# Performance work log

Hardware: AMD Instinct MI355X
Metric: run time of the kernel (lower is better)

Reference implementation:

```python
import jax, jax.numpy as jnp
import numpy as np

NUM_EMBEDDINGS = 8192
EMBEDDING_DIM = 128
COMMITMENT_COST = 0.02


def _l2_normalize(x, axis=-1, eps=1e-12):
    # matches torch F.normalize: x / max(||x||, eps)
    n = jnp.sqrt(jnp.sum(x * x, axis=axis, keepdims=True))
    return x / jnp.maximum(n, eps)


def setup_inputs() -> dict:
    key = jax.random.key(0)
    k1, k2 = jax.random.split(key)
    inputs = jax.random.normal(k1, (16, 128, 2048), dtype=jnp.float32)  # [B, D, T]
    lim = 1.0 / NUM_EMBEDDINGS
    codebook = jax.random.uniform(k2, (NUM_EMBEDDINGS, EMBEDDING_DIM),
                                  dtype=jnp.float32, minval=-lim, maxval=lim)
    return {"inputs": inputs, "codebook": codebook}


def reference(inputs, codebook):
    # inputs: [B, D, T] -> [B, T, D]
    x = jnp.transpose(inputs, (0, 2, 1))
    B, T, D = x.shape
    flat = x.reshape(-1, D)                      # [N, D]
    flat_n = _l2_normalize(flat, axis=1)         # [N, D]
    emb_n = _l2_normalize(codebook, axis=1)      # [K, D]
    # cosine-style distance: 2 - 2 * <x_hat, e_hat>
    distances = 2.0 - 2.0 * jnp.einsum('nd,kd->nk', flat_n, emb_n)  # [N, K]
    encoding_indices = jnp.argmin(distances, axis=1)[:, None]       # [N, 1]
    # (dead-code revival is a training-time RNG side effect on the codebook;
    #  eval path / reference math skips it)
    quantized = codebook[encoding_indices[:, 0]].reshape(B, T, D)   # [B, T, D]
    sg = jax.lax.stop_gradient
    e_latent_loss = jnp.mean((sg(quantized) - x) ** 2)
    q_latent_loss = jnp.mean((quantized - sg(x)) ** 2)
    loss = q_latent_loss + COMMITMENT_COST * e_latent_loss
    # straight-through estimator
    quantized_st = x + sg(quantized - x)
    out = jnp.transpose(quantized_st, (0, 2, 1))  # back to [B, D, T]
    return loss, out, encoding_indices
```

## Files before the change

### kernel.cpp

```cpp
#include <hip/hip_runtime.h>
#include <hip/hip_bf16.h>

#define NROWS 32768
#define KCODES 8192
#define DDIM 128
#define TT 2048
#define ETOT 4194304

typedef __attribute__((ext_vector_type(8))) _Float16 f16x8;
typedef __attribute__((ext_vector_type(4))) float f32x4;

__device__ __forceinline__ float pk(float v, int p) {
    return __int_as_float((__float_as_int(v) & 0xFFFFE000) | p);
}

__device__ __forceinline__ void async16(char* lds_uniform, const char* g_perlane) {
    __builtin_amdgcn_global_load_lds(
        (const __attribute__((address_space(1))) unsigned int*)g_perlane,
        (__attribute__((address_space(3))) unsigned int*)lds_uniform,
        16, 0, 0);
}

#define SYNC2 asm volatile("s_waitcnt vmcnt(2) lgkmcnt(0)\n\ts_barrier" ::: "memory")
#define SYNC0 asm volatile("s_waitcnt vmcnt(0) lgkmcnt(0)\n\ts_barrier" ::: "memory")

__global__ void k_prep(const float* __restrict__ cb, _Float16* __restrict__ eh,
                       const float* __restrict__ in, _Float16* __restrict__ xh) {
    __shared__ float tb[64][65];
    int bid = blockIdx.x;
    if (bid < 2048) {
        int w = (bid * blockDim.x + threadIdx.x) >> 6;
        int l = threadIdx.x & 63;
        if (w >= KCODES) return;
        const float* row = cb + (long)w * DDIM;
        float v0 = row[l], v1 = row[l + 64];
        float ss = v0 * v0 + v1 * v1;
#pragma unroll
        for (int s = 1; s < 64; s <<= 1) ss += __shfl_xor(ss, s, 64);
        float inv = 1.0f / fmaxf(sqrtf(ss), 1e-12f);
        int tile = w >> 4, c = w & 15;
#pragma unroll
        for (int e = 0; e < 2; e++) {
            int d = l + e * 64;
            float v = (e ? v1 : v0) * inv;
            int ks = d >> 5, kq = (d >> 3) & 3, dr = d & 7;
            long off = (long)tile * 2048 + ks * 512 + (kq * 16 + c) * 8 + dr;
            eh[off] = (_Float16)v;
        }
    } else {
        bid -= 2048;
        int tt0 = (bid & 31) * 64;
        int dd0 = ((bid >> 5) & 1) * 64;
        int b = bid >> 6;
        const float* base = in + (long)b * DDIM * TT;
        int tl = threadIdx.x & 63;
        int dg = threadIdx.x >> 6;
#pragma unroll
        for (int i = 0; i < 16; i++) {
            int dd = dg + i * 4;
            tb[dd][tl] = base[(long)(dd0 + dd) * TT + tt0 + tl];
        }
        __syncthreads();
        int dl = threadIdx.x & 63;
        int tg = threadIdx.x >> 6;
#pragma unroll
        for (int i = 0; i < 16; i++) {
            int t = tg + i * 4;
            long n = (long)b * TT + tt0 + t;
            xh[n * DDIM + dd0 + dl] = (_Float16)tb[dl][t];
        }
    }
}

__device__ __forceinline__ void mfma4i(const char* buf, int l,
                                       const f16x8 (&bx)[4][4], f32x4 (&acc)[4]) {
    const f32x4 Z = {0.f, 0.f, 0.f, 0.f};
    f16x8 ah[4];
#pragma unroll
    for (int ks = 0; ks < 4; ks++)
        ah[ks] = *(const f16x8*)(buf + ks * 1024 + l * 16);
    __builtin_amdgcn_s_setprio(1);
#pragma unroll
    for (int nf = 0; nf < 4; nf++)
        acc[nf] = __builtin_amdgcn_mfma_f32_16x16x32_f16(ah[0], bx[nf][0], Z, 0, 0, 0);
#pragma unroll
    for (int ks = 1; ks < 4; ks++)
#pragma unroll
        for (int nf = 0; nf < 4; nf++)
            acc[nf] = __builtin_amdgcn_mfma_f32_16x16x32_f16(ah[ks], bx[nf][ks], acc[nf], 0, 0, 0);
    __builtin_amdgcn_s_setprio(0);
}

__device__ __forceinline__ void sel4(const f32x4 (&acc)[4], int PP,
                                     float (&t1)[4], float (&t2)[4], float (&u1)[4]) {
#pragma unroll
    for (int nf = 0; nf < 4; nf++) {
        f32x4 a = acc[nf];
        float s0 = pk(a[0], PP),     s1 = pk(a[1], PP - 1);
        float s2 = pk(a[2], PP - 2), s3 = pk(a[3], PP - 3);
        float h01 = fmaxf(s0, s1), l01 = fminf(s0, s1);
        float h23 = fmaxf(s2, s3), l23 = fminf(s2, s3);
        float m1 = fmaxf(h01, h23);
        float m2 = fmaxf(fminf(h01, h23), fmaxf(l01, l23));
        float n1 = fminf(t1[nf], m1); t1[nf] = fmaxf(t1[nf], m1);
        t2[nf] = fmaxf(t2[nf], n1);
        u1[nf] = fmaxf(u1[nf], m2);
    }
}

__global__ __launch_bounds__(256, 3) void k_main(const _Float16* __restrict__ xh,
                                                 const _Float16* __restrict__ eh,
                                                 int* __restrict__ cand) {
    extern __shared__ char lds[];
    const int tid = threadIdx.x;
    const int l = tid & 63;
    const int w = tid >> 6;
    const int e8 = blockIdx.x & 7;
    const int rb = blockIdx.x >> 3;
    const int col = l & 15, kq = l >> 4;
    const long rbase = (long)rb * 256;

    f16x8 bx[4][4];
#pragma unroll
    for (int nf = 0; nf < 4; nf++) {
        long n = rbase + w * 64 + nf * 16 + col;
#pragma unroll
        for (int ks = 0; ks < 4; ks++)
            bx[nf][ks] = *(const f16x8*)(xh + n * DDIM + ks * 32 + kq * 8);
    }

    const float NEG = __int_as_float(0xFF800000);
    float t1[4], t2[4], u1[4];
#pragma unroll
    for (int i = 0; i < 4; i++) { t1[i] = t2[i] = u1[i] = NEG; }

    int P = 8191 - (e8 * 1024 + kq * 4);

    const char* gsrc = (const char*)eh + (long)e8 * 262144 + w * 1024 + l * 16;
    char* b0 = lds;
    char* b1 = lds + 8192;
    char* b2 = lds + 16384;

    async16(b0 + w * 1024, gsrc);
    async16(b0 + 4096 + w * 1024, gsrc + 4096);
    async16(b1 + w * 1024, gsrc + 8192);
    async16(b1 + 4096 + w * 1024, gsrc + 12288);

    f32x4 accA[4], accB[4];
    int PA, PB;

    SYNC2;
    async16(b2 + w * 1024, gsrc + 2 * 8192);
    async16(b2 + 4096 + w * 1024, gsrc + 2 * 8192 + 4096);
    mfma4i(b0, l, bx, accA); PA = P; P -= 16;
    mfma4i(b0 + 4096, l, bx, accB); PB = P; P -= 16;
    sel4(accA, PA, t1, t2, u1);
    { char* tp = b0; b0 = b1; b1 = b2; b2 = tp; }

    for (int p = 1; p <= 30; ++p) {
        SYNC2;
        if (p < 30) {
            async16(b2 + w * 1024, gsrc + (long)(p + 2) * 8192);
            async16(b2 + 4096 + w * 1024, gsrc + (long)(p + 2) * 8192 + 4096);
        }
        mfma4i(b0, l, bx, accA); PA = P; P -= 16;
        sel4(accB, PB, t1, t2, u1);
        mfma4i(b0 + 4096, l, bx, accB); PB = P; P -= 16;
        sel4(accA, PA, t1, t2, u1);
        { char* tp = b0; b0 = b1; b1 = b2; b2 = tp; }
    }
    SYNC0;
    mfma4i(b0, l, bx, accA); PA = P; P -= 16;
    sel4(accB, PB, t1, t2, u1);
    mfma4i(b0 + 4096, l, bx, accB); PB = P;
    sel4(accA, PA, t1, t2, u1);
    sel4(accB, PB, t1, t2, u1);

    __syncthreads();
    float* mrg = (float*)lds;
#pragma unroll
    for (int nf = 0; nf < 4; nf++) {
        int row = w * 64 + nf * 16 + col;
        int e = kq * 3;
        mrg[row * 13 + e + 0] = t1[nf];
        mrg[row * 13 + e + 1] = t2[nf];
        mrg[row * 13 + e + 2] = u1[nf];
    }
    __syncthreads();
    {
        float s1 = NEG, s2 = NEG;
#pragma unroll 4
        for (int e = 0; e < 12; e++) {
            float v = mrg[tid * 13 + e];
            float a1 = fminf(s1, v); s1 = fmaxf(s1, v);
            s2 = fmaxf(s2, a1);
        }
        long n = rbase + tid;
        int* cp = cand + n * 16 + e8 * 2;
        cp[0] = 8191 - (__float_as_int(s1) & 0x1FFF);
        cp[1] = 8191 - (__float_as_int(s2) & 0x1FFF);
    }
}

__global__ void k_rf(const float* __restrict__ in, const float* __restrict__ cb,
                     const int* __restrict__ cand, float* __restrict__ out,
                     float* __restrict__ idx_f, double* __restrict__ part) {
    __shared__ float xs[16][132];
    __shared__ int sbi[16];
    __shared__ double sd[256];
    const int tid = threadIdx.x;
    const int n0 = blockIdx.x * 16;
    const int b = n0 >> 11, t0 = n0 & 2047;

    {
        int d = tid >> 1, h = tid & 1;
        const float* src = in + ((long)b * DDIM + d) * TT + t0 + h * 8;
        float4 v0 = *(const float4*)src;
        float4 v1 = *(const float4*)(src + 4);
#pragma unroll
        for (int j = 0; j < 4; j++) {
            xs[h * 8 + j][d] = ((const float*)&v0)[j];
            xs[h * 8 + 4 + j][d] = ((const float*)&v1)[j];
        }
    }
    __syncthreads();

    {
        int r = tid >> 4, k = tid & 15;
        int n = n0 + r;
        int c = cand[n * 16 + k];
        const float4* e = (const float4*)(cb + (long)c * DDIM);
        double dot = 0.0, nrm = 0.0;
        for (int d4 = 0; d4 < 32; d4++) {
            float4 q = e[d4];
#pragma unroll
            for (int j = 0; j < 4; j++) {
                double xd = (double)xs[r][d4 * 4 + j];
                double f = (double)((const float*)&q)[j];
                dot += xd * f;
                nrm += f * f;
            }
        }
        double sv = dot / fmax(sqrt(nrm), 1e-12);
#pragma unroll
        for (int s = 1; s < 16; s <<= 1) {
            double osv = __shfl_xor(sv, s, 64);
            int oc = __shfl_xor(c, s, 64);
            if (osv > sv || (osv == sv && oc < c)) { sv = osv; c = oc; }
        }
        if (k == 0) {
            sbi[r] = c;
            idx_f[n] = (float)c;
        }
    }
    __syncthreads();

    {
        int d = tid >> 1, h = tid & 1;
        float* ob = out + ((long)b * DDIM + d) * TT + t0 + h * 8;
        double acc = 0.0;
        float ov[8];
#pragma unroll
        for (int j = 0; j < 8; j++) {
            int rr = h * 8 + j;
            float xv = xs[rr][d];
            float qv = cb[(long)sbi[rr] * DDIM + d];
            float diff = qv - xv;
            ov[j] = xv + diff;
            acc += (double)diff * (double)diff;
        }
        *(float4*)ob = make_float4(ov[0], ov[1], ov[2], ov[3]);
        *(float4*)(ob + 4) = make_float4(ov[4], ov[5], ov[6], ov[7]);
        sd[tid] = acc;
    }
    __syncthreads();
    for (int s = 128; s > 0; s >>= 1) {
        if (tid < s) sd[tid] += sd[tid + s];
        __syncthreads();
    }
    if (tid == 0) part[blockIdx.x] = sd[0];
}

__global__ void k_loss_final(const double* __restrict__ part, int np,
                             float* __restrict__ loss) {
    __shared__ double sd[256];
    double a = 0.0;
    for (int i = threadIdx.x; i < np; i += 256) a += part[i];
    sd[threadIdx.x] = a;
    __syncthreads();
    for (int s = 128; s > 0; s >>= 1) {
        if (threadIdx.x < s) sd[threadIdx.x] += sd[threadIdx.x + s];
        __syncthreads();
    }
    if (threadIdx.x == 0) {
        float m = (float)(sd[0] / (double)ETOT);
        loss[0] = m + 0.02f * m;
    }
}

extern "C" void kernel_launch(void* const* d_in, const int* in_sizes, int n_in,
                              void* d_out, int out_size, void* d_ws, size_t ws_size,
                              hipStream_t stream) {
    const float* inputs = (const float*)d_in[0];
    const float* cb     = (const float*)d_in[1];
    float* outf = (float*)d_out;

    char* ws = (char*)d_ws;
    _Float16* xh = (_Float16*)ws; ws += (long)NROWS * DDIM * 2;
    _Float16* eh = (_Float16*)ws; ws += (long)KCODES * DDIM * 2;
    int* cand    = (int*)ws;      ws += (long)NROWS * 16 * 4;
    double* part = (double*)ws;   ws += 2048 * 8;

    k_prep<<<dim3(3072), dim3(256), 0, stream>>>(cb, eh, inputs, xh);
    k_main<<<dim3(1024), dim3(256), 24576, stream>>>(xh, eh, cand);
    k_rf<<<dim3(2048), dim3(256), 0, stream>>>(inputs, cb, cand, outf + 1,
                                               outf + 1 + (long)ETOT, part);
    k_loss_final<<<dim3(1), dim3(256), 0, stream>>>(part, 2048, outf);
}
```

Baseline: 135.1 us.

## Drop double-buffered accumulators to raise occupancy, vectorize rerank x loads

The main distance kernel drops the A/B accumulator ping-pong, which overlapped MFMA of one half-tile with top-k selection of the other, and uses a single accumulator set in a uniform 32-iteration loop. Launch bounds rise from 3 to 4 waves per SIMD to match the lower register pressure. Selection now depends directly on the preceding MFMA results, so instruction-level overlap is traded for more resident wavefronts. The rerank kernel also reads the shared-memory x row as float4 instead of scalar loads.

```diff
diff --git a/kernel.cpp b/kernel.cpp
--- a/kernel.cpp
+++ b/kernel.cpp
@@ -108,7 +108,7 @@
     }
 }
 
-__global__ __launch_bounds__(256, 3) void k_main(const _Float16* __restrict__ xh,
+__global__ __launch_bounds__(256, 4) void k_main(const _Float16* __restrict__ xh,
                                                  const _Float16* __restrict__ eh,
                                                  int* __restrict__ cand) {
     extern __shared__ char lds[];
@@ -146,35 +146,24 @@
     async16(b1 + w * 1024, gsrc + 8192);
     async16(b1 + 4096 + w * 1024, gsrc + 12288);
 
-    f32x4 accA[4], accB[4];
-    int PA, PB;
-
-    SYNC2;
-    async16(b2 + w * 1024, gsrc + 2 * 8192);
-    async16(b2 + 4096 + w * 1024, gsrc + 2 * 8192 + 4096);
-    mfma4i(b0, l, bx, accA); PA = P; P -= 16;
-    mfma4i(b0 + 4096, l, bx, accB); PB = P; P -= 16;
-    sel4(accA, PA, t1, t2, u1);
-    { char* tp = b0; b0 = b1; b1 = b2; b2 = tp; }
-
-    for (int p = 1; p <= 30; ++p) {
-        SYNC2;
+    f32x4 acc[4];
+
+    for (int p = 0; p < 32; ++p) {
         if (p < 30) {
+            SYNC2;
             async16(b2 + w * 1024, gsrc + (long)(p + 2) * 8192);
             async16(b2 + 4096 + w * 1024, gsrc + (long)(p + 2) * 8192 + 4096);
-        }
-        mfma4i(b0, l, bx, accA); PA = P; P -= 16;
-        sel4(accB, PB, t1, t2, u1);
-        mfma4i(b0 + 4096, l, bx, accB); PB = P; P -= 16;
-        sel4(accA, PA, t1, t2, u1);
-        { char* tp = b0; b0 = b1; b1 = b2; b2 = tp; }
-    }
-    SYNC0;
-    mfma4i(b0, l, bx, accA); PA = P; P -= 16;
-    sel4(accB, PB, t1, t2, u1);
-    mfma4i(b0 + 4096, l, bx, accB); PB = P;
-    sel4(accA, PA, t1, t2, u1);
-    sel4(accB, PB, t1, t2, u1);
+        } else if (p == 30) {
+            SYNC2;
+        } else {
+            SYNC0;
+        }
+        mfma4i(b0, l, bx, acc);
+        sel4(acc, P, t1, t2, u1); P -= 16;
+        mfma4i(b0 + 4096, l, bx, acc);
+        sel4(acc, P, t1, t2, u1); P -= 16;
+        char* tp = b0; b0 = b1; b1 = b2; b2 = tp;
+    }
 
     __syncthreads();
     float* mrg = (float*)lds;
@@ -230,12 +219,14 @@
         int n = n0 + r;
         int c = cand[n * 16 + k];
         const float4* e = (const float4*)(cb + (long)c * DDIM);
+        const float4* xr = (const float4*)&xs[r][0];
         double dot = 0.0, nrm = 0.0;
         for (int d4 = 0; d4 < 32; d4++) {
             float4 q = e[d4];
+            float4 xv = xr[d4];
 #pragma unroll
             for (int j = 0; j < 4; j++) {
-                double xd = (double)xs[r][d4 * 4 + j];
+                double xd = (double)((const float*)&xv)[j];
                 double f = (double)((const float*)&q)[j];
                 dot += xd * f;
                 nrm += f * f;
```

New measurement: 136.8 us. About the same (+1.2%).
